# Optimization experiments

Hardware: AMD Instinct MI355X
Metric: run time of the kernel (lower is better)

The kernel has to match this reference:

```python
import jax, jax.numpy as jnp
import numpy as np
import math

D_MODEL, N_HEADS, D_FF = 1024, 16, 4096
B, S = 2, 2048
EPS = 1e-8
NEG = -1e9


def setup_inputs() -> dict:
    key = jax.random.key(0)
    ks = jax.random.split(key, 8)
    sc = 0.02
    return {
        "x": jax.random.normal(ks[0], (B, S, D_MODEL), dtype=jnp.float32),
        "mask": jnp.ones((B, 1, 1, S), dtype=jnp.int32),
        "Wq": jax.random.normal(ks[1], (D_MODEL, D_MODEL), dtype=jnp.float32) * sc,
        "bq": jnp.zeros((D_MODEL,), dtype=jnp.float32),
        "Wk": jax.random.normal(ks[2], (D_MODEL, D_MODEL), dtype=jnp.float32) * sc,
        "bk": jnp.zeros((D_MODEL,), dtype=jnp.float32),
        "Wv": jax.random.normal(ks[3], (D_MODEL, D_MODEL), dtype=jnp.float32) * sc,
        "bv": jnp.zeros((D_MODEL,), dtype=jnp.float32),
        "Wo": jax.random.normal(ks[4], (D_MODEL, D_MODEL), dtype=jnp.float32) * sc,
        "bo": jnp.zeros((D_MODEL,), dtype=jnp.float32),
        "W1": jax.random.normal(ks[5], (D_FF, D_MODEL), dtype=jnp.float32) * sc,
        "b1": jnp.zeros((D_FF,), dtype=jnp.float32),
        "W2": jax.random.normal(ks[6], (D_MODEL, D_FF), dtype=jnp.float32) * sc,
        "b2": jnp.zeros((D_MODEL,), dtype=jnp.float32),
        "g1": jnp.ones((1, 1, 1), dtype=jnp.float32),
        "be1": jnp.zeros((1, 1, 1), dtype=jnp.float32),
        "g2": jnp.ones((1, 1, 1), dtype=jnp.float32),
        "be2": jnp.zeros((1, 1, 1), dtype=jnp.float32),
    }


def _layernorm(x, gamma, beta):
    # Matches torch: mean / unbiased std (ddof=1), eps added to std (not var)
    mean = jnp.mean(x, axis=-1, keepdims=True)
    std = jnp.std(x, axis=-1, keepdims=True, ddof=1)
    return gamma * (x - mean) / (std + EPS) + beta


def reference(x, mask, Wq, bq, Wk, bk, Wv, bv, Wo, bo, W1, b1, W2, b2, g1, be1, g2, be2):
    dk = D_MODEL // N_HEADS

    # --- pre-norm self-attention + residual ---
    h = _layernorm(x, g1, be1)
    q = h @ Wq.T + bq
    k = h @ Wk.T + bk
    v = h @ Wv.T + bv
    # [B,S,D] -> [B,H,S,dk]
    q = q.reshape(B, S, N_HEADS, dk).transpose(0, 2, 1, 3)
    k = k.reshape(B, S, N_HEADS, dk).transpose(0, 2, 1, 3)
    v = v.reshape(B, S, N_HEADS, dk).transpose(0, 2, 1, 3)
    scores = jnp.einsum('bhqd,bhkd->bhqk', q, k) / math.sqrt(dk)
    scores = jnp.where(mask == 0, NEG, scores)
    attn = jax.nn.softmax(scores, axis=-1)
    ctx = jnp.einsum('bhqk,bhkd->bhqd', attn, v)  # [B,H,S,dk]
    ctx = ctx.transpose(0, 2, 1, 3).reshape(B, S, D_MODEL)
    x = x + (ctx @ Wo.T + bo)

    # --- pre-norm FFN + residual ---
    h2 = _layernorm(x, g2, be2)
    f = jax.nn.relu(h2 @ W1.T + b1) @ W2.T + b2
    return x + f
```

## Files before the change

kernel.cpp:

```cpp
#include <hip/hip_runtime.h>
#include <math.h>

#define D_MODEL 1024
#define N_HEADS 16
#define DK      64
#define D_FF    4096
#define BB      2
#define SS      2048
#define ROWS    (BB * SS)
#define EPS     1e-8f
#define NEG     -1e9f
#define QSCALE  0.1803368801111f

union F4 { float4 v; float f[4]; };

typedef __attribute__((ext_vector_type(8))) short   bf16x8;
typedef __attribute__((ext_vector_type(4))) float   f32x4;

__device__ __forceinline__ unsigned short f2bf(float f) {
    union { float f; unsigned u; } a; a.f = f;
    unsigned r = a.u + 0x7FFFu + ((a.u >> 16) & 1u);
    return (unsigned short)(r >> 16);
}

__device__ __forceinline__ float exp2_fast(float x) {
    float r;
    asm("v_exp_f32 %0, %1" : "=v"(r) : "v"(x));
    return r;
}

__device__ __forceinline__ unsigned cvt_pk_bf16(float lo, float hi) {
    unsigned r;
    asm("v_cvt_pk_bf16_f32 %0, %1, %2" : "=v"(r) : "v"(lo), "v"(hi));
    return r;
}

__device__ __forceinline__ void gload16(const void* g, void* l) {
    __builtin_amdgcn_global_load_lds(
        (const __attribute__((address_space(1))) unsigned int*)g,
        (__attribute__((address_space(3))) unsigned int*)l, 16, 0, 0);
}

__global__ __launch_bounds__(256) void ln_bf16_kernel(const float* __restrict__ x,
                                                      const float* __restrict__ g,
                                                      const float* __restrict__ be,
                                                      unsigned short* __restrict__ out) {
    __shared__ float sm[8];
    const int row = blockIdx.x;
    float4 v = ((const float4*)(x + (size_t)row * D_MODEL))[threadIdx.x];

    float s = v.x + v.y + v.z + v.w;
#pragma unroll
    for (int o = 32; o; o >>= 1) s += __shfl_xor(s, o);
    const int wid = threadIdx.x >> 6, lane = threadIdx.x & 63;
    if (lane == 0) sm[wid] = s;
    __syncthreads();
    const float mean = (sm[0] + sm[1] + sm[2] + sm[3]) * (1.0f / D_MODEL);

    const float dx = v.x - mean, dy = v.y - mean, dz = v.z - mean, dw = v.w - mean;
    float sq = dx * dx + dy * dy + dz * dz + dw * dw;
#pragma unroll
    for (int o = 32; o; o >>= 1) sq += __shfl_xor(sq, o);
    if (lane == 0) sm[4 + wid] = sq;
    __syncthreads();
    const float var = (sm[4] + sm[5] + sm[6] + sm[7]) * (1.0f / (D_MODEL - 1));
    const float inv = 1.0f / (sqrtf(var) + EPS);
    const float g0 = g[0], b0 = be[0];

    ushort4 o4;
    o4.x = f2bf(g0 * dx * inv + b0);
    o4.y = f2bf(g0 * dy * inv + b0);
    o4.z = f2bf(g0 * dz * inv + b0);
    o4.w = f2bf(g0 * dw * inv + b0);
    ((ushort4*)(out + (size_t)row * D_MODEL))[threadIdx.x] = o4;
}

__global__ __launch_bounds__(256) void cast_bf16_kernel(const float* __restrict__ in,
                                                        unsigned short* __restrict__ out,
                                                        int n4) {
    const int i = blockIdx.x * 256 + threadIdx.x;
    if (i < n4) {
        float4 v = ((const float4*)in)[i];
        ushort4 o = { f2bf(v.x), f2bf(v.y), f2bf(v.z), f2bf(v.w) };
        ((ushort4*)out)[i] = o;
    }
}

__global__ __launch_bounds__(256) void mask_prep(const int* __restrict__ mask,
                                                 float* __restrict__ mbias,
                                                 int* __restrict__ tflag) {
    const int i = blockIdx.x * 256 + threadIdx.x;
    const int m = mask[i];
    mbias[i] = m ? 0.0f : NEG;
    unsigned long long z = __ballot(m == 0);
    if ((threadIdx.x & 63) == 0) tflag[i >> 6] = (z != 0ull) ? 1 : 0;
}

template <bool RELU, bool RES, bool OUTBF, bool BROW>
__device__ __forceinline__ void gemm_core(const unsigned short* __restrict__ A,
                                          const unsigned short* __restrict__ B,
                                          const float* __restrict__ bias,
                                          const float* __restrict__ res,
                                          void* __restrict__ Cout,
                                          int M, int N, int K, float scale,
                                          int bm, int bn,
                                          unsigned short* As, unsigned short* Bs) {
    const int tid  = threadIdx.x;
    const int lane = tid & 63;
    const int wv   = tid >> 6;
    const int wr   = wv >> 1, wc = wv & 1;
    const int lr   = lane & 15, lq = lane >> 4;

    f32x4 acc[4][4];
#pragma unroll
    for (int m = 0; m < 4; ++m)
#pragma unroll
        for (int n = 0; n < 4; ++n)
            acc[m][n] = (f32x4){0.f, 0.f, 0.f, 0.f};

    const int srow = wv * 32 + (lane >> 2);
    const int scol = (lane & 3) * 8;

    auto stage = [&](int buf, int k0) {
        unsigned short* ab = As + buf * 4096;
        unsigned short* bb = Bs + buf * 4096;
        gload16(A + (size_t)(bm + srow) * K + k0 + scol,      &ab[(wv * 32) * 32]);
        gload16(A + (size_t)(bm + srow + 16) * K + k0 + scol, &ab[(wv * 32 + 16) * 32]);
        gload16(B + (size_t)(bn + srow) * K + k0 + scol,      &bb[(wv * 32) * 32]);
        gload16(B + (size_t)(bn + srow + 16) * K + k0 + scol, &bb[(wv * 32 + 16) * 32]);
    };

    const int T = K >> 5;
    stage(0, 0);
    __syncthreads();

    for (int t = 0; t < T; ++t) {
        const int cur = t & 1;
        if (t + 1 < T) stage(cur ^ 1, (t + 1) << 5);
        __builtin_amdgcn_sched_barrier(0);

        const unsigned short* ab = As + cur * 4096;
        const unsigned short* bb = Bs + cur * 4096;
        bf16x8 af[4], bf[4];
#pragma unroll
        for (int m = 0; m < 4; ++m)
            af[m] = *(const bf16x8*)&ab[(wr * 64 + m * 16 + lr) * 32 + lq * 8];
#pragma unroll
        for (int n = 0; n < 4; ++n)
            bf[n] = *(const bf16x8*)&bb[(wc * 64 + n * 16 + lr) * 32 + lq * 8];

#pragma unroll
        for (int m = 0; m < 4; ++m)
#pragma unroll
            for (int n = 0; n < 4; ++n)
                acc[m][n] = __builtin_amdgcn_mfma_f32_16x16x32_bf16(af[m], bf[n], acc[m][n], 0, 0, 0);

        __syncthreads();
    }

#pragma unroll
    for (int n = 0; n < 4; ++n) {
        const int col = bn + wc * 64 + n * 16 + lr;
        const float bcol = BROW ? 0.0f : bias[col];
#pragma unroll
        for (int m = 0; m < 4; ++m) {
#pragma unroll
            for (int r = 0; r < 4; ++r) {
                const int row = bm + wr * 64 + m * 16 + lq * 4 + r;
                float v = acc[m][n][r] + (BROW ? bias[row] : bcol);
                v *= scale;
                if (RELU) v = fmaxf(v, 0.0f);
                if (RES)  v += res[(size_t)row * N + col];
                if (OUTBF) ((unsigned short*)Cout)[(size_t)row * N + col] = f2bf(v);
                else       ((float*)Cout)[(size_t)row * N + col] = v;
            }
        }
    }
}

template <bool RELU, bool RES, bool OUTBF, bool BROW>
__global__ __launch_bounds__(256) void gemm_bf16(const unsigned short* __restrict__ A,
                                                 const unsigned short* __restrict__ B,
                                                 const float* __restrict__ bias,
                                                 const float* __restrict__ res,
                                                 void* __restrict__ Cout,
                                                 int M, int N, int K, float scale) {
    __shared__ unsigned short As[2 * 4096];
    __shared__ unsigned short Bs[2 * 4096];
    gemm_core<RELU, RES, OUTBF, BROW>(A, B, bias, res, Cout, M, N, K, scale,
                                      blockIdx.y * 128, blockIdx.x * 128, As, Bs);
}

__global__ __launch_bounds__(256) void qkv_fused(const unsigned short* __restrict__ h,
                                                 const unsigned short* __restrict__ Wq,
                                                 const unsigned short* __restrict__ Wk,
                                                 const unsigned short* __restrict__ Wv,
                                                 const float* __restrict__ bq,
                                                 const float* __restrict__ bk,
                                                 const float* __restrict__ bv,
                                                 unsigned short* __restrict__ qo,
                                                 unsigned short* __restrict__ ko,
                                                 unsigned short* __restrict__ vto) {
    __shared__ unsigned short As[2 * 4096];
    __shared__ unsigned short Bs[2 * 4096];
    const int id = blockIdx.x;
    const int op = id >> 8;
    const int t  = id & 255;
    if (op == 0) {
        gemm_core<false, false, true, false>(h, Wq, bq, nullptr, qo,
            ROWS, D_MODEL, D_MODEL, QSCALE, (t >> 3) * 128, (t & 7) * 128, As, Bs);
    } else if (op == 1) {
        gemm_core<false, false, true, false>(h, Wk, bk, nullptr, ko,
            ROWS, D_MODEL, D_MODEL, 1.0f, (t >> 3) * 128, (t & 7) * 128, As, Bs);
    } else {
        gemm_core<false, false, true, true>(Wv, h, bv, nullptr, vto,
            D_MODEL, ROWS, D_MODEL, 1.0f, (t >> 5) * 128, (t & 31) * 128, As, Bs);
    }
}

__global__ __launch_bounds__(256) void attn_mfma(const unsigned short* __restrict__ Q,
                                                 const unsigned short* __restrict__ K,
                                                 const unsigned short* __restrict__ Vt,
                                                 const float* __restrict__ mbias,
                                                 const int* __restrict__ tflag,
                                                 unsigned short* __restrict__ O) {
    __shared__ unsigned short Ks[64][68];
    __shared__ unsigned short Vs[64][68];
    __shared__ unsigned short Ps[64][68];

    const int bh = blockIdx.x, qt = blockIdx.y;
    const int b = bh >> 4, h = bh & 15;
    const int q0 = qt * 64;
    const int tid = threadIdx.x;
    const int w = tid >> 6, lane = tid & 63;
    const int lr = lane & 15, lq = lane >> 4;

    const size_t qkbase = (size_t)b * SS * D_MODEL + (size_t)h * DK;
    const int tok0 = b * SS;
    const float* mb = mbias + (size_t)b * SS;
    const int* tf = tflag + b * (SS / 64);

    const unsigned short* qp = Q + qkbase + (size_t)(q0 + w * 16 + lr) * D_MODEL;
    const bf16x8 qf0 = *(const bf16x8*)(qp + lq * 8);
    const bf16x8 qf1 = *(const bf16x8*)(qp + 32 + lq * 8);

    const int sr = tid >> 3, sch = tid & 7;
    bf16x8 kreg0, kreg1, vreg0, vreg1;
    {
        const unsigned short* kp = K + qkbase + (size_t)sr * D_MODEL + sch * 8;
        kreg0 = *(const bf16x8*)(kp);
        kreg1 = *(const bf16x8*)(kp + 32 * D_MODEL);
        const unsigned short* vp = Vt + (size_t)(h * DK + sr) * ROWS + tok0 + sch * 8;
        vreg0 = *(const bf16x8*)(vp);
        vreg1 = *(const bf16x8*)(vp + 32 * ROWS);
    }

    f32x4 acc_o[4];
#pragma unroll
    for (int n = 0; n < 4; ++n) acc_o[n] = (f32x4){0.f, 0.f, 0.f, 0.f};
    float m_run = -1e30f, l_run = 0.0f;

    for (int kt = 0; kt < SS / 64; ++kt) {
        __syncthreads();
        *(bf16x8*)&Ks[sr][sch * 8]      = kreg0;
        *(bf16x8*)&Ks[sr + 32][sch * 8] = kreg1;
        *(bf16x8*)&Vs[sr][sch * 8]      = vreg0;
        *(bf16x8*)&Vs[sr + 32][sch * 8] = vreg1;
        __syncthreads();

        if (kt + 1 < SS / 64) {
            const int k1 = (kt + 1) * 64;
            const unsigned short* kp = K + qkbase + (size_t)(k1 + sr) * D_MODEL + sch * 8;
            kreg0 = *(const bf16x8*)(kp);
            kreg1 = *(const bf16x8*)(kp + 32 * D_MODEL);
            const unsigned short* vp = Vt + (size_t)(h * DK + sr) * ROWS + tok0 + k1 + sch * 8;
            vreg0 = *(const bf16x8*)(vp);
            vreg1 = *(const bf16x8*)(vp + 32 * ROWS);
        }

        f32x4 sa[4];
#pragma unroll
        for (int n = 0; n < 4; ++n) sa[n] = (f32x4){0.f, 0.f, 0.f, 0.f};
#pragma unroll
        for (int n = 0; n < 4; ++n) {
            bf16x8 kf0 = *(const bf16x8*)&Ks[n * 16 + lr][lq * 8];
            bf16x8 kf1 = *(const bf16x8*)&Ks[n * 16 + lr][32 + lq * 8];
            sa[n] = __builtin_amdgcn_mfma_f32_16x16x32_bf16(kf0, qf0, sa[n], 0, 0, 0);
            sa[n] = __builtin_amdgcn_mfma_f32_16x16x32_bf16(kf1, qf1, sa[n], 0, 0, 0);
        }

        if (tf[kt]) {
#pragma unroll
            for (int n = 0; n < 4; ++n) {
                F4 m4; m4.v = *(const float4*)&mb[kt * 64 + n * 16 + lq * 4];
#pragma unroll
                for (int r = 0; r < 4; ++r) sa[n][r] += m4.f[r];
            }
        }

        float pmax = sa[0][0];
#pragma unroll
        for (int n = 0; n < 4; ++n)
#pragma unroll
            for (int r = 0; r < 4; ++r) pmax = fmaxf(pmax, sa[n][r]);
        pmax = fmaxf(pmax, __shfl_xor(pmax, 16));
        pmax = fmaxf(pmax, __shfl_xor(pmax, 32));
        const float mn = fmaxf(m_run, pmax);
        const float sc = exp2_fast(m_run - mn);
        m_run = mn;
        float rs = 0.0f;
#pragma unroll
        for (int n = 0; n < 4; ++n)
#pragma unroll
            for (int r = 0; r < 4; ++r) {
                const float p = exp2_fast(sa[n][r] - mn);
                sa[n][r] = p;
                rs += p;
            }
        rs += __shfl_xor(rs, 16);
        rs += __shfl_xor(rs, 32);
        l_run = l_run * sc + rs;
#pragma unroll
        for (int n = 0; n < 4; ++n) {
            acc_o[n][0] *= sc; acc_o[n][1] *= sc; acc_o[n][2] *= sc; acc_o[n][3] *= sc;
        }

#pragma unroll
        for (int n = 0; n < 4; ++n) {
            uint2 u;
            u.x = cvt_pk_bf16(sa[n][0], sa[n][1]);
            u.y = cvt_pk_bf16(sa[n][2], sa[n][3]);
            *(uint2*)&Ps[w * 16 + lr][n * 16 + lq * 4] = u;
        }

#pragma unroll
        for (int c = 0; c < 2; ++c) {
            bf16x8 pf = *(const bf16x8*)&Ps[w * 16 + lr][c * 32 + lq * 8];
#pragma unroll
            for (int n = 0; n < 4; ++n) {
                bf16x8 vf = *(const bf16x8*)&Vs[n * 16 + lr][c * 32 + lq * 8];
                acc_o[n] = __builtin_amdgcn_mfma_f32_16x16x32_bf16(vf, pf, acc_o[n], 0, 0, 0);
            }
        }
    }

    const float invl = 1.0f / l_run;
    unsigned short* orow = O + qkbase + (size_t)(q0 + w * 16 + lr) * D_MODEL;
#pragma unroll
    for (int n = 0; n < 4; ++n) {
        ushort4 o;
        o.x = f2bf(acc_o[n][0] * invl);
        o.y = f2bf(acc_o[n][1] * invl);
        o.z = f2bf(acc_o[n][2] * invl);
        o.w = f2bf(acc_o[n][3] * invl);
        *(ushort4*)(orow + n * 16 + lq * 4) = o;
    }
}

extern "C" void kernel_launch(void* const* d_in, const int* in_sizes, int n_in,
                              void* d_out, int out_size, void* d_ws, size_t ws_size,
                              hipStream_t stream) {
    const float* x   = (const float*)d_in[0];
    const int*   msk = (const int*)d_in[1];
    const float* Wq  = (const float*)d_in[2];
    const float* bq  = (const float*)d_in[3];
    const float* Wk  = (const float*)d_in[4];
    const float* bk  = (const float*)d_in[5];
    const float* Wv  = (const float*)d_in[6];
    const float* bv  = (const float*)d_in[7];
    const float* Wo  = (const float*)d_in[8];
    const float* bo  = (const float*)d_in[9];
    const float* W1  = (const float*)d_in[10];
    const float* b1  = (const float*)d_in[11];
    const float* W2  = (const float*)d_in[12];
    const float* b2  = (const float*)d_in[13];
    const float* g1  = (const float*)d_in[14];
    const float* be1 = (const float*)d_in[15];
    const float* g2  = (const float*)d_in[16];
    const float* be2 = (const float*)d_in[17];
    float* out = (float*)d_out;

    char* w = (char*)d_ws;
    unsigned short* h_bf   = (unsigned short*)w; w += (size_t)ROWS * D_MODEL * 2;
    unsigned short* qb_bf  = (unsigned short*)w; w += (size_t)ROWS * D_MODEL * 2;
    unsigned short* kb_bf  = (unsigned short*)w; w += (size_t)ROWS * D_MODEL * 2;
    unsigned short* vt_bf  = (unsigned short*)w; w += (size_t)ROWS * D_MODEL * 2;
    unsigned short* ctx_bf = (unsigned short*)w; w += (size_t)ROWS * D_MODEL * 2;
    float* xat             = (float*)w;          w += (size_t)ROWS * D_MODEL * 4;
    unsigned short* h2_bf  = (unsigned short*)w; w += (size_t)ROWS * D_MODEL * 2;
    unsigned short* ff1_bf = (unsigned short*)w; w += (size_t)ROWS * D_FF * 2;
    unsigned short* Wq_bf  = (unsigned short*)w; w += (size_t)D_MODEL * D_MODEL * 2;
    unsigned short* Wk_bf  = (unsigned short*)w; w += (size_t)D_MODEL * D_MODEL * 2;
    unsigned short* Wv_bf  = (unsigned short*)w; w += (size_t)D_MODEL * D_MODEL * 2;
    unsigned short* Wo_bf  = (unsigned short*)w; w += (size_t)D_MODEL * D_MODEL * 2;
    unsigned short* W1_bf  = (unsigned short*)w; w += (size_t)D_FF * D_MODEL * 2;
    unsigned short* W2_bf  = (unsigned short*)w; w += (size_t)D_FF * D_MODEL * 2;
    float* mbias           = (float*)w;          w += (size_t)ROWS * 4;
    int* tflag             = (int*)w;            w += (size_t)(BB * SS / 64) * 4;

    const dim3 blk(256);
    const int nD = D_MODEL * D_MODEL / 4;
    const int nF = D_FF * D_MODEL / 4;
    cast_bf16_kernel<<<(nD + 255) / 256, blk, 0, stream>>>(Wq, Wq_bf, nD);
    cast_bf16_kernel<<<(nD + 255) / 256, blk, 0, stream>>>(Wk, Wk_bf, nD);
    cast_bf16_kernel<<<(nD + 255) / 256, blk, 0, stream>>>(Wv, Wv_bf, nD);
    cast_bf16_kernel<<<(nD + 255) / 256, blk, 0, stream>>>(Wo, Wo_bf, nD);
    cast_bf16_kernel<<<(nF + 255) / 256, blk, 0, stream>>>(W1, W1_bf, nF);
    cast_bf16_kernel<<<(nF + 255) / 256, blk, 0, stream>>>(W2, W2_bf, nF);
    mask_prep<<<ROWS / 256, blk, 0, stream>>>(msk, mbias, tflag);

    ln_bf16_kernel<<<ROWS, blk, 0, stream>>>(x, g1, be1, h_bf);

    qkv_fused<<<768, blk, 0, stream>>>(h_bf, Wq_bf, Wk_bf, Wv_bf, bq, bk, bv,
                                       qb_bf, kb_bf, vt_bf);

    attn_mfma<<<dim3(BB * N_HEADS, SS / 64), blk, 0, stream>>>(qb_bf, kb_bf, vt_bf,
                                                               mbias, tflag, ctx_bf);

    const dim3 gD(D_MODEL / 128, ROWS / 128);
    const dim3 gF(D_FF / 128, ROWS / 128);
    gemm_bf16<false, true, false, false><<<gD, blk, 0, stream>>>(ctx_bf, Wo_bf, bo, x, xat, ROWS, D_MODEL, D_MODEL, 1.0f);

    ln_bf16_kernel<<<ROWS, blk, 0, stream>>>(xat, g2, be2, h2_bf);

    gemm_bf16<true, false, true, false><<<gF, blk, 0, stream>>>(h2_bf, W1_bf, b1, nullptr, ff1_bf, ROWS, D_FF, D_MODEL, 1.0f);
    gemm_bf16<false, true, false, false><<<gD, blk, 0, stream>>>(ff1_bf, W2_bf, b2, xat, out, ROWS, D_MODEL, D_FF, 1.0f);
}
```

Before: 426.3 us.

## Double-buffer attention K/V, defer softmax rescale, add N64 GEMM, fuse weight casts

Several independent changes. The six weight-cast launches are merged into one grid-stride kernel. The attention kernel double-buffers the K/V tiles in shared memory, which drops one barrier per iteration, and wraps its MFMA blocks in s_setprio. Its online-softmax rescale is skipped unless the running max grows past a threshold. The two N=1024 GEMMs (Wo and W2) now use a new 128x64 tile kernel that launches twice as many blocks for better CU occupancy, at the cost of lower per-block data reuse.

```diff
diff --git a/kernel.cpp b/kernel.cpp
--- a/kernel.cpp
+++ b/kernel.cpp
@@ -11,6 +11,7 @@
 #define EPS     1e-8f
 #define NEG     -1e9f
 #define QSCALE  0.1803368801111f
+#define DEFER_THR 11.541560327f
 
 union F4 { float4 v; float f[4]; };
 
@@ -75,14 +76,38 @@
     ((ushort4*)(out + (size_t)row * D_MODEL))[threadIdx.x] = o4;
 }
 
-__global__ __launch_bounds__(256) void cast_bf16_kernel(const float* __restrict__ in,
-                                                        unsigned short* __restrict__ out,
-                                                        int n4) {
-    const int i = blockIdx.x * 256 + threadIdx.x;
-    if (i < n4) {
-        float4 v = ((const float4*)in)[i];
+__global__ __launch_bounds__(256) void cast_all(const float* __restrict__ s0,
+                                                const float* __restrict__ s1,
+                                                const float* __restrict__ s2,
+                                                const float* __restrict__ s3,
+                                                const float* __restrict__ s4,
+                                                const float* __restrict__ s5,
+                                                unsigned short* __restrict__ d0,
+                                                unsigned short* __restrict__ d1,
+                                                unsigned short* __restrict__ d2,
+                                                unsigned short* __restrict__ d3,
+                                                unsigned short* __restrict__ d4,
+                                                unsigned short* __restrict__ d5) {
+    const int ND4 = D_MODEL * D_MODEL / 4;
+    const int NF4 = D_FF * D_MODEL / 4;
+    const int total = 4 * ND4 + 2 * NF4;
+    for (int i = blockIdx.x * 256 + threadIdx.x; i < total; i += gridDim.x * 256) {
+        const float* s; unsigned short* d; int off;
+        if (i < 4 * ND4) {
+            const int w = i >> 18;
+            off = i & (ND4 - 1);
+            s = (w == 0) ? s0 : (w == 1) ? s1 : (w == 2) ? s2 : s3;
+            d = (w == 0) ? d0 : (w == 1) ? d1 : (w == 2) ? d2 : d3;
+        } else {
+            const int j = i - 4 * ND4;
+            const int w = j >> 20;
+            off = j & (NF4 - 1);
+            s = w ? s5 : s4;
+            d = w ? d5 : d4;
+        }
+        float4 v = ((const float4*)s)[off];
         ushort4 o = { f2bf(v.x), f2bf(v.y), f2bf(v.z), f2bf(v.w) };
-        ((ushort4*)out)[i] = o;
+        ((ushort4*)d)[off] = o;
     }
 }
 
@@ -189,6 +214,91 @@
     __shared__ unsigned short Bs[2 * 4096];
     gemm_core<RELU, RES, OUTBF, BROW>(A, B, bias, res, Cout, M, N, K, scale,
                                       blockIdx.y * 128, blockIdx.x * 128, As, Bs);
+}
+
+template <bool RELU, bool RES, bool OUTBF>
+__global__ __launch_bounds__(256) void gemm_n64(const unsigned short* __restrict__ A,
+                                                const unsigned short* __restrict__ B,
+                                                const float* __restrict__ bias,
+                                                const float* __restrict__ res,
+                                                void* __restrict__ Cout,
+                                                int M, int N, int K, float scale) {
+    __shared__ unsigned short As[2 * 4096];
+    __shared__ unsigned short Bs[2 * 2048];
+
+    const int bm = blockIdx.y * 128;
+    const int bn = blockIdx.x * 64;
+    const int tid  = threadIdx.x;
+    const int lane = tid & 63;
+    const int wv   = tid >> 6;
+    const int wr   = wv >> 1, wc = wv & 1;
+    const int lr   = lane & 15, lq = lane >> 4;
+
+    f32x4 acc[4][2];
+#pragma unroll
+    for (int m = 0; m < 4; ++m)
+#pragma unroll
+        for (int n = 0; n < 2; ++n)
+            acc[m][n] = (f32x4){0.f, 0.f, 0.f, 0.f};
+
+    const int sra = wv * 32 + (lane >> 2);
+    const int srb = wv * 16 + (lane >> 2);
+    const int scol = (lane & 3) * 8;
+
+    auto stage = [&](int buf, int k0) {
+        unsigned short* ab = As + buf * 4096;
+        unsigned short* bb = Bs + buf * 2048;
+        gload16(A + (size_t)(bm + sra) * K + k0 + scol,      &ab[(wv * 32) * 32]);
+        gload16(A + (size_t)(bm + sra + 16) * K + k0 + scol, &ab[(wv * 32 + 16) * 32]);
+        gload16(B + (size_t)(bn + srb) * K + k0 + scol,      &bb[(wv * 16) * 32]);
+    };
+
+    const int T = K >> 5;
+    stage(0, 0);
+    __syncthreads();
+
+    for (int t = 0; t < T; ++t) {
+        const int cur = t & 1;
+        if (t + 1 < T) stage(cur ^ 1, (t + 1) << 5);
+        __builtin_amdgcn_sched_barrier(0);
+
+        const unsigned short* ab = As + cur * 4096;
+        const unsigned short* bb = Bs + cur * 2048;
+        bf16x8 af[4], bf[2];
+#pragma unroll
+        for (int m = 0; m < 4; ++m)
+            af[m] = *(const bf16x8*)&ab[(wr * 64 + m * 16 + lr) * 32 + lq * 8];
+#pragma unroll
+        for (int n = 0; n < 2; ++n)
+            bf[n] = *(const bf16x8*)&bb[(wc * 32 + n * 16 + lr) * 32 + lq * 8];
+
+#pragma unroll
+        for (int m = 0; m < 4; ++m)
+#pragma unroll
+            for (int n = 0; n < 2; ++n)
+                acc[m][n] = __builtin_amdgcn_mfma_f32_16x16x32_bf16(af[m], bf[n], acc[m][n], 0, 0, 0);
+
+        __syncthreads();
+    }
+
+#pragma unroll
+    for (int n = 0; n < 2; ++n) {
+        const int col = bn + wc * 32 + n * 16 + lr;
+        const float bcol = bias[col];
+#pragma unroll
+        for (int m = 0; m < 4; ++m) {
+#pragma unroll
+            for (int r = 0; r < 4; ++r) {
+                const int row = bm + wr * 64 + m * 16 + lq * 4 + r;
+                float v = acc[m][n][r] + bcol;
+                v *= scale;
+                if (RELU) v = fmaxf(v, 0.0f);
+                if (RES)  v += res[(size_t)row * N + col];
+                if (OUTBF) ((unsigned short*)Cout)[(size_t)row * N + col] = f2bf(v);
+                else       ((float*)Cout)[(size_t)row * N + col] = v;
+            }
+        }
+    }
 }
 
 __global__ __launch_bounds__(256) void qkv_fused(const unsigned short* __restrict__ h,
@@ -224,8 +334,8 @@
                                                  const float* __restrict__ mbias,
                                                  const int* __restrict__ tflag,
                                                  unsigned short* __restrict__ O) {
-    __shared__ unsigned short Ks[64][68];
-    __shared__ unsigned short Vs[64][68];
+    __shared__ unsigned short Ks[2][64][68];
+    __shared__ unsigned short Vs[2][64][68];
     __shared__ unsigned short Ps[64][68];
 
     const int bh = blockIdx.x, qt = blockIdx.y;
@@ -254,21 +364,21 @@
         vreg0 = *(const bf16x8*)(vp);
         vreg1 = *(const bf16x8*)(vp + 32 * ROWS);
     }
+    *(bf16x8*)&Ks[0][sr][sch * 8]      = kreg0;
+    *(bf16x8*)&Ks[0][sr + 32][sch * 8] = kreg1;
+    *(bf16x8*)&Vs[0][sr][sch * 8]      = vreg0;
+    *(bf16x8*)&Vs[0][sr + 32][sch * 8] = vreg1;
+    __syncthreads();
 
     f32x4 acc_o[4];
 #pragma unroll
     for (int n = 0; n < 4; ++n) acc_o[n] = (f32x4){0.f, 0.f, 0.f, 0.f};
     float m_run = -1e30f, l_run = 0.0f;
 
-    for (int kt = 0; kt < SS / 64; ++kt) {
-        __syncthreads();
-        *(bf16x8*)&Ks[sr][sch * 8]      = kreg0;
-        *(bf16x8*)&Ks[sr + 32][sch * 8] = kreg1;
-        *(bf16x8*)&Vs[sr][sch * 8]      = vreg0;
-        *(bf16x8*)&Vs[sr + 32][sch * 8] = vreg1;
-        __syncthreads();
-
-        if (kt + 1 < SS / 64) {
+    const int NT = SS / 64;
+    for (int kt = 0; kt < NT; ++kt) {
+        const int cur = kt & 1;
+        if (kt + 1 < NT) {
             const int k1 = (kt + 1) * 64;
             const unsigned short* kp = K + qkbase + (size_t)(k1 + sr) * D_MODEL + sch * 8;
             kreg0 = *(const bf16x8*)(kp);
@@ -281,13 +391,15 @@
         f32x4 sa[4];
 #pragma unroll
         for (int n = 0; n < 4; ++n) sa[n] = (f32x4){0.f, 0.f, 0.f, 0.f};
+        __builtin_amdgcn_s_setprio(1);
 #pragma unroll
         for (int n = 0; n < 4; ++n) {
-            bf16x8 kf0 = *(const bf16x8*)&Ks[n * 16 + lr][lq * 8];
-            bf16x8 kf1 = *(const bf16x8*)&Ks[n * 16 + lr][32 + lq * 8];
+            bf16x8 kf0 = *(const bf16x8*)&Ks[cur][n * 16 + lr][lq * 8];
+            bf16x8 kf1 = *(const bf16x8*)&Ks[cur][n * 16 + lr][32 + lq * 8];
             sa[n] = __builtin_amdgcn_mfma_f32_16x16x32_bf16(kf0, qf0, sa[n], 0, 0, 0);
             sa[n] = __builtin_amdgcn_mfma_f32_16x16x32_bf16(kf1, qf1, sa[n], 0, 0, 0);
         }
+        __builtin_amdgcn_s_setprio(0);
 
         if (tf[kt]) {
 #pragma unroll
@@ -305,25 +417,29 @@
             for (int r = 0; r < 4; ++r) pmax = fmaxf(pmax, sa[n][r]);
         pmax = fmaxf(pmax, __shfl_xor(pmax, 16));
         pmax = fmaxf(pmax, __shfl_xor(pmax, 32));
-        const float mn = fmaxf(m_run, pmax);
-        const float sc = exp2_fast(m_run - mn);
-        m_run = mn;
+
+        if (!__all(pmax - m_run <= DEFER_THR)) {
+            const float mn = fmaxf(m_run, pmax);
+            const float sc = exp2_fast(m_run - mn);
+            m_run = mn;
+            l_run *= sc;
+#pragma unroll
+            for (int n = 0; n < 4; ++n) {
+                acc_o[n][0] *= sc; acc_o[n][1] *= sc; acc_o[n][2] *= sc; acc_o[n][3] *= sc;
+            }
+        }
         float rs = 0.0f;
 #pragma unroll
         for (int n = 0; n < 4; ++n)
 #pragma unroll
             for (int r = 0; r < 4; ++r) {
-                const float p = exp2_fast(sa[n][r] - mn);
+                const float p = exp2_fast(sa[n][r] - m_run);
                 sa[n][r] = p;
                 rs += p;
             }
         rs += __shfl_xor(rs, 16);
         rs += __shfl_xor(rs, 32);
-        l_run = l_run * sc + rs;
-#pragma unroll
-        for (int n = 0; n < 4; ++n) {
-            acc_o[n][0] *= sc; acc_o[n][1] *= sc; acc_o[n][2] *= sc; acc_o[n][3] *= sc;
-        }
+        l_run += rs;
 
 #pragma unroll
         for (int n = 0; n < 4; ++n) {
@@ -333,15 +449,25 @@
             *(uint2*)&Ps[w * 16 + lr][n * 16 + lq * 4] = u;
         }
 
+        __builtin_amdgcn_s_setprio(1);
 #pragma unroll
         for (int c = 0; c < 2; ++c) {
             bf16x8 pf = *(const bf16x8*)&Ps[w * 16 + lr][c * 32 + lq * 8];
 #pragma unroll
             for (int n = 0; n < 4; ++n) {
-                bf16x8 vf = *(const bf16x8*)&Vs[n * 16 + lr][c * 32 + lq * 8];
+                bf16x8 vf = *(const bf16x8*)&Vs[cur][n * 16 + lr][c * 32 + lq * 8];
                 acc_o[n] = __builtin_amdgcn_mfma_f32_16x16x32_bf16(vf, pf, acc_o[n], 0, 0, 0);
             }
         }
+        __builtin_amdgcn_s_setprio(0);
+
+        if (kt + 1 < NT) {
+            *(bf16x8*)&Ks[cur ^ 1][sr][sch * 8]      = kreg0;
+            *(bf16x8*)&Ks[cur ^ 1][sr + 32][sch * 8] = kreg1;
+            *(bf16x8*)&Vs[cur ^ 1][sr][sch * 8]      = vreg0;
+            *(bf16x8*)&Vs[cur ^ 1][sr + 32][sch * 8] = vreg1;
+        }
+        __syncthreads();
     }
 
     const float invl = 1.0f / l_run;
@@ -399,14 +525,8 @@
     int* tflag             = (int*)w;            w += (size_t)(BB * SS / 64) * 4;
 
     const dim3 blk(256);
-    const int nD = D_MODEL * D_MODEL / 4;
-    const int nF = D_FF * D_MODEL / 4;
-    cast_bf16_kernel<<<(nD + 255) / 256, blk, 0, stream>>>(Wq, Wq_bf, nD);
-    cast_bf16_kernel<<<(nD + 255) / 256, blk, 0, stream>>>(Wk, Wk_bf, nD);
-    cast_bf16_kernel<<<(nD + 255) / 256, blk, 0, stream>>>(Wv, Wv_bf, nD);
-    cast_bf16_kernel<<<(nD + 255) / 256, blk, 0, stream>>>(Wo, Wo_bf, nD);
-    cast_bf16_kernel<<<(nF + 255) / 256, blk, 0, stream>>>(W1, W1_bf, nF);
-    cast_bf16_kernel<<<(nF + 255) / 256, blk, 0, stream>>>(W2, W2_bf, nF);
+    cast_all<<<2048, blk, 0, stream>>>(Wq, Wk, Wv, Wo, W1, W2,
+                                       Wq_bf, Wk_bf, Wv_bf, Wo_bf, W1_bf, W2_bf);
     mask_prep<<<ROWS / 256, blk, 0, stream>>>(msk, mbias, tflag);
 
     ln_bf16_kernel<<<ROWS, blk, 0, stream>>>(x, g1, be1, h_bf);
@@ -417,12 +537,14 @@
     attn_mfma<<<dim3(BB * N_HEADS, SS / 64), blk, 0, stream>>>(qb_bf, kb_bf, vt_bf,
                                                                mbias, tflag, ctx_bf);
 
-    const dim3 gD(D_MODEL / 128, ROWS / 128);
-    const dim3 gF(D_FF / 128, ROWS / 128);
-    gemm_bf16<false, true, false, false><<<gD, blk, 0, stream>>>(ctx_bf, Wo_bf, bo, x, xat, ROWS, D_MODEL, D_MODEL, 1.0f);
+    gemm_n64<false, true, false><<<dim3(D_MODEL / 64, ROWS / 128), blk, 0, stream>>>(
+        ctx_bf, Wo_bf, bo, x, xat, ROWS, D_MODEL, D_MODEL, 1.0f);
 
     ln_bf16_kernel<<<ROWS, blk, 0, stream>>>(xat, g2, be2, h2_bf);
 
-    gemm_bf16<true, false, true, false><<<gF, blk, 0, stream>>>(h2_bf, W1_bf, b1, nullptr, ff1_bf, ROWS, D_FF, D_MODEL, 1.0f);
-    gemm_bf16<false, true, false, false><<<gD, blk, 0, stream>>>(ff1_bf, W2_bf, b2, xat, out, ROWS, D_MODEL, D_FF, 1.0f);
-}
+    gemm_bf16<true, false, true, false><<<dim3(D_FF / 128, ROWS / 128), blk, 0, stream>>>(
+        h2_bf, W1_bf, b1, nullptr, ff1_bf, ROWS, D_FF, D_MODEL, 1.0f);
+
+    gemm_n64<false, true, false><<<dim3(D_MODEL / 64, ROWS / 128), blk, 0, stream>>>(
+        ff1_bf, W2_bf, b2, xat, out, ROWS, D_MODEL, D_FF, 1.0f);
+}
```

Measured after the change: 405.8 us. -4.8%, faster.
